# Kernel optimization log

Hardware: AMD Instinct MI355X
Metric: run time of the kernel (lower is better)

The kernel has to match this reference:

```python
import jax, jax.numpy as jnp
import numpy as np

NUM_SAMPLES = 128      # num_samples_per_ray
HIST_PAD = 0.01        # histogram_padding
EPS = 1e-5             # eps
N_RAYS = 262144
N_COARSE = 64


def setup_inputs() -> dict:
    key = jax.random.key(0)
    k1, k2 = jax.random.split(key, 2)
    weights = jax.random.uniform(k1, (N_RAYS, N_COARSE, 1), dtype=jnp.float32)
    # monotonically increasing bins along each ray (cumsum of positive deltas)
    deltas = jax.random.uniform(k2, (N_RAYS, N_COARSE + 1), dtype=jnp.float32) * 0.1 + 0.01
    t = jnp.cumsum(deltas, axis=-1)
    bins = t[:, :N_COARSE, None]        # [R, N, 1]
    max_bin = t[:, N_COARSE:]           # [R, 1]
    return {"weights": weights, "bins": bins, "max_bin": max_bin}


def reference(weights, bins, max_bin):
    # eval-mode PDFSampler (deterministic u = linspace + 0.5/num_bins)
    w = weights[..., 0] + HIST_PAD                      # [R, N]
    w_sum = jnp.sum(w, axis=-1, keepdims=True)          # [R, 1]
    padding = jnp.maximum(EPS - w_sum, 0.0)             # relu(eps - sum)
    w = w + padding / w.shape[-1]
    pdf = w / (w_sum + padding)
    cdf = jnp.minimum(jnp.cumsum(pdf, axis=-1), 1.0)    # clamp_max(1)
    cdf = jnp.concatenate([jnp.zeros_like(cdf[..., :1]), cdf], axis=-1)  # [R, N+1]

    num_bins = NUM_SAMPLES + 1
    u = jnp.linspace(0.0, 1.0 - 1.0 / num_bins, num_bins, dtype=cdf.dtype) + 0.5 / num_bins
    u = jnp.broadcast_to(u, (cdf.shape[0], num_bins))   # [R, S+1]

    existing_bins = jnp.concatenate([bins[..., 0], max_bin], axis=-1)  # [R, N+1]

    idx = jax.vmap(lambda c, uu: jnp.searchsorted(c, uu, side='right'))(cdf, u)
    last = cdf.shape[-1] - 1
    below = jnp.clip(idx - 1, 0, last)
    above = jnp.clip(idx, 0, last)

    cdf_g0 = jnp.take_along_axis(cdf, below, axis=-1)
    cdf_g1 = jnp.take_along_axis(cdf, above, axis=-1)
    bins_g0 = jnp.take_along_axis(existing_bins, below, axis=-1)
    bins_g1 = jnp.take_along_axis(existing_bins, above, axis=-1)

    denom = cdf_g1 - cdf_g0
    safe = jnp.where(denom > 0, denom, 1.0)
    ts = jnp.clip(jnp.where(denom > 0, (u - cdf_g0) / safe, 0.0), 0.0, 1.0)
    new_bins = bins_g0 + ts * (bins_g1 - bins_g0)       # [R, S+1]

    # include_original: merge with existing bins, sort, drop last
    new_bins = jnp.sort(jnp.concatenate([existing_bins, new_bins], axis=-1), axis=-1)[..., :-1]
    # [R, N + S + 1] = [R, 193]; caller splits into bins=new_bins[..., :-1, None], max_bin=new_bins[..., -1:]
    return new_bins
```

## Files before the change

kernel.cpp:

```cpp
#include <hip/hip_runtime.h>


constexpr int kNCoarse = 64;
constexpr int kNumU    = 129;
constexpr int kNOut    = 193;
constexpr int kWaves   = 8;
constexpr int kBlock   = kWaves * 64;
constexpr int kBlockF  = kWaves * kNOut;
constexpr int kBlockV4 = kBlockF / 4;

typedef float f32x4 __attribute__((ext_vector_type(4)));

#define DPP_UPD_F(oldv, srcv, ctrl, rmask, bctrl)                             \
  __int_as_float(__builtin_amdgcn_update_dpp(                                 \
      __float_as_int(oldv), __float_as_int(srcv), (ctrl), (rmask), 0xF, (bctrl)))

__global__ __launch_bounds__(kBlock) void pdf_sampler_kernel(
    const float* __restrict__ weights,
    const float* __restrict__ bins,
    const float* __restrict__ max_bin,
    float* __restrict__ out,
    int n_rays)
{
    const int tid  = threadIdx.x;
    const int lane = tid & 63;
    const int wid  = tid >> 6;
    const int ray  = blockIdx.x * kWaves + wid;

    __shared__ __align__(16) float s_m[kBlockF];

    if (ray < n_rays) {
        const float w  = weights[(size_t)ray * kNCoarse + lane] + 0.01f;
        const float b0 = bins[(size_t)ray * kNCoarse + lane];
        const float mb = max_bin[ray];

        float c = w;
        c += DPP_UPD_F(0.0f, c, 0x111, 0xF, true);
        c += DPP_UPD_F(0.0f, c, 0x112, 0xF, true);
        c += DPP_UPD_F(0.0f, c, 0x114, 0xF, true);
        c += DPP_UPD_F(0.0f, c, 0x118, 0xF, true);
        c += DPP_UPD_F(0.0f, c, 0x142, 0xA, false);
        c += DPP_UPD_F(0.0f, c, 0x143, 0xC, false);

        const float ws        = __int_as_float(__builtin_amdgcn_readlane(__float_as_int(c), 63));
        const float padding   = fmaxf(1e-5f - ws, 0.0f);
        const float inv_total = __builtin_amdgcn_rcpf(ws + padding);
        const float pad64     = padding * (1.0f / 64.0f);

        const float c1 = fminf((c + (float)(lane + 1) * pad64) * inv_total, 1.0f);
        const float c0 = DPP_UPD_F(0.0f, c1, 0x138, 0xF, true);
        const float b1 = DPP_UPD_F(mb,   b0, 0x130, 0xF, false);

        const float kInv = 1.0f / 129.0f, kHalf = 0.5f / 129.0f;
        int js = (int)ceilf(fmaf(c0, 129.0f, -0.5f));
        js = min(max(js, 0), kNumU);
        {
            const float um1 = fmaf((float)(js - 1), kInv, kHalf);
            const float u0e = fmaf((float)js,       kInv, kHalf);
            if (js > 0 && um1 >= c0)           js -= 1;
            else if (js < kNumU && u0e < c0)   js += 1;
        }
        const int js_next = __builtin_amdgcn_update_dpp(kNumU, js, 0x130, 0xF, 0xF, false);

        const float denom  = c1 - c0;
        const float rdenom = (denom > 0.0f) ? __builtin_amdgcn_rcpf(denom) : 0.0f;
        const float dbin   = b1 - b0;
        const float u0     = fmaf((float)js, kInv, kHalf);
        const float t0     = fminf(fmaxf((u0 - c0) * rdenom, 0.0f), 1.0f);
        float       val    = fmaf(t0, dbin, b0);
        const float step   = kInv * rdenom * dbin;

        float* mrow = s_m + wid * kNOut;
        mrow[lane + js] = b0;
        for (int j = js; j < js_next; ++j) {
            mrow[j + lane + 1] = val;
            val += step;
        }
    }

    __syncthreads();

    {
        const int raysHere = min(n_rays - blockIdx.x * kWaves, kWaves);
        if (raysHere > 0) {
            const int nf = raysHere * kNOut;
            float* obase = out + (size_t)blockIdx.x * kBlockF;
            if (tid < kBlockV4) {
                const int off = tid * 4;
                if (off + 3 < nf) {
                    const f32x4 v = *reinterpret_cast<const f32x4*>(&s_m[off]);
                    __builtin_nontemporal_store(v, reinterpret_cast<f32x4*>(&obase[off]));
                } else {
                    for (int k = off; k < nf; ++k)
                        __builtin_nontemporal_store(s_m[k], &obase[k]);
                }
            }
        }
    }
}

extern "C" void kernel_launch(void* const* d_in, const int* in_sizes, int n_in,
                              void* d_out, int out_size, void* d_ws, size_t ws_size,
                              hipStream_t stream) {
    const float* weights = (const float*)d_in[0];
    const float* bins    = (const float*)d_in[1];
    const float* max_bin = (const float*)d_in[2];
    float* out = (float*)d_out;
    const int n_rays = in_sizes[2];
    const int blocks = (n_rays + kWaves - 1) / kWaves;
    pdf_sampler_kernel<<<blocks, kBlock, 0, stream>>>(weights, bins, max_bin, out, n_rays);
}
```

Before: 55.70 us.

## Make kernel persistent with register prefetch and double-buffered LDS staging

Launches a fixed grid of 4096 blocks, and each block loops over a contiguous range of 8-ray groups. The next group's weights, bins and max_bin are loaded into registers while the current group is computed, and the output staging buffer in shared memory is double-buffered so only one barrier is needed per iteration. The aim is to cut block launch overhead and hide global load latency. In exchange, each block keeps fewer loads in flight per wave and carries a longer serial chain, and LDS use per block doubles.

```diff
diff --git a/kernel.cpp b/kernel.cpp
--- a/kernel.cpp
+++ b/kernel.cpp
@@ -6,8 +6,9 @@
 constexpr int kNOut    = 193;
 constexpr int kWaves   = 8;
 constexpr int kBlock   = kWaves * 64;
-constexpr int kBlockF  = kWaves * kNOut;
-constexpr int kBlockV4 = kBlockF / 4;
+constexpr int kGroupF  = kWaves * kNOut;
+constexpr int kGroupV4 = kGroupF / 4;
+constexpr int kGrid    = 4096;
 
 typedef float f32x4 __attribute__((ext_vector_type(4)));
 
@@ -25,74 +26,101 @@
     const int tid  = threadIdx.x;
     const int lane = tid & 63;
     const int wid  = tid >> 6;
-    const int ray  = blockIdx.x * kWaves + wid;
 
-    __shared__ __align__(16) float s_m[kBlockF];
+    const int nGroups = (n_rays + kWaves - 1) / kWaves;
+    const int T       = (nGroups + kGrid - 1) / kGrid;
+    const int g0      = blockIdx.x * T;
+    const int gEnd    = min(g0 + T, nGroups);
+    if (g0 >= nGroups) return;
 
-    if (ray < n_rays) {
-        const float w  = weights[(size_t)ray * kNCoarse + lane] + 0.01f;
-        const float b0 = bins[(size_t)ray * kNCoarse + lane];
-        const float mb = max_bin[ray];
+    __shared__ __align__(16) float s_m[2][kGroupF];
 
-        float c = w;
-        c += DPP_UPD_F(0.0f, c, 0x111, 0xF, true);
-        c += DPP_UPD_F(0.0f, c, 0x112, 0xF, true);
-        c += DPP_UPD_F(0.0f, c, 0x114, 0xF, true);
-        c += DPP_UPD_F(0.0f, c, 0x118, 0xF, true);
-        c += DPP_UPD_F(0.0f, c, 0x142, 0xA, false);
-        c += DPP_UPD_F(0.0f, c, 0x143, 0xC, false);
-
-        const float ws        = __int_as_float(__builtin_amdgcn_readlane(__float_as_int(c), 63));
-        const float padding   = fmaxf(1e-5f - ws, 0.0f);
-        const float inv_total = __builtin_amdgcn_rcpf(ws + padding);
-        const float pad64     = padding * (1.0f / 64.0f);
-
-        const float c1 = fminf((c + (float)(lane + 1) * pad64) * inv_total, 1.0f);
-        const float c0 = DPP_UPD_F(0.0f, c1, 0x138, 0xF, true);
-        const float b1 = DPP_UPD_F(mb,   b0, 0x130, 0xF, false);
-
-        const float kInv = 1.0f / 129.0f, kHalf = 0.5f / 129.0f;
-        int js = (int)ceilf(fmaf(c0, 129.0f, -0.5f));
-        js = min(max(js, 0), kNumU);
-        {
-            const float um1 = fmaf((float)(js - 1), kInv, kHalf);
-            const float u0e = fmaf((float)js,       kInv, kHalf);
-            if (js > 0 && um1 >= c0)           js -= 1;
-            else if (js < kNumU && u0e < c0)   js += 1;
-        }
-        const int js_next = __builtin_amdgcn_update_dpp(kNumU, js, 0x130, 0xF, 0xF, false);
-
-        const float denom  = c1 - c0;
-        const float rdenom = (denom > 0.0f) ? __builtin_amdgcn_rcpf(denom) : 0.0f;
-        const float dbin   = b1 - b0;
-        const float u0     = fmaf((float)js, kInv, kHalf);
-        const float t0     = fminf(fmaxf((u0 - c0) * rdenom, 0.0f), 1.0f);
-        float       val    = fmaf(t0, dbin, b0);
-        const float step   = kInv * rdenom * dbin;
-
-        float* mrow = s_m + wid * kNOut;
-        mrow[lane + js] = b0;
-        for (int j = js; j < js_next; ++j) {
-            mrow[j + lane + 1] = val;
-            val += step;
+    float w = 0.0f, b0 = 0.0f, mb = 0.0f;
+    {
+        const int ray = g0 * kWaves + wid;
+        if (ray < n_rays) {
+            w  = weights[(size_t)ray * kNCoarse + lane];
+            b0 = bins[(size_t)ray * kNCoarse + lane];
+            mb = max_bin[ray];
         }
     }
 
-    __syncthreads();
+    int p = 0;
+    for (int g = g0; g < gEnd; ++g, p ^= 1) {
+        const int ray = g * kWaves + wid;
 
-    {
-        const int raysHere = min(n_rays - blockIdx.x * kWaves, kWaves);
-        if (raysHere > 0) {
+        if (ray < n_rays) {
+            const float wp = w + 0.01f;
+
+            float c = wp;
+            c += DPP_UPD_F(0.0f, c, 0x111, 0xF, true);
+            c += DPP_UPD_F(0.0f, c, 0x112, 0xF, true);
+            c += DPP_UPD_F(0.0f, c, 0x114, 0xF, true);
+            c += DPP_UPD_F(0.0f, c, 0x118, 0xF, true);
+            c += DPP_UPD_F(0.0f, c, 0x142, 0xA, false);
+            c += DPP_UPD_F(0.0f, c, 0x143, 0xC, false);
+
+            const float ws        = __int_as_float(__builtin_amdgcn_readlane(__float_as_int(c), 63));
+            const float padding   = fmaxf(1e-5f - ws, 0.0f);
+            const float inv_total = __builtin_amdgcn_rcpf(ws + padding);
+            const float pad64     = padding * (1.0f / 64.0f);
+
+            const float c1 = fminf((c + (float)(lane + 1) * pad64) * inv_total, 1.0f);
+            const float c0 = DPP_UPD_F(0.0f, c1, 0x138, 0xF, true);
+            const float b1 = DPP_UPD_F(mb,   b0, 0x130, 0xF, false);
+
+            const float kInv = 1.0f / 129.0f, kHalf = 0.5f / 129.0f;
+            int js = (int)ceilf(fmaf(c0, 129.0f, -0.5f));
+            js = min(max(js, 0), kNumU);
+            {
+                const float um1 = fmaf((float)(js - 1), kInv, kHalf);
+                const float u0e = fmaf((float)js,       kInv, kHalf);
+                if (js > 0 && um1 >= c0)           js -= 1;
+                else if (js < kNumU && u0e < c0)   js += 1;
+            }
+            const int js_next = __builtin_amdgcn_update_dpp(kNumU, js, 0x130, 0xF, 0xF, false);
+
+            const float denom  = c1 - c0;
+            const float rdenom = (denom > 0.0f) ? __builtin_amdgcn_rcpf(denom) : 0.0f;
+            const float dbin   = b1 - b0;
+            const float u0     = fmaf((float)js, kInv, kHalf);
+            const float t0     = fminf(fmaxf((u0 - c0) * rdenom, 0.0f), 1.0f);
+            float       val    = fmaf(t0, dbin, b0);
+            const float step   = kInv * rdenom * dbin;
+
+            float* mrow = s_m[p] + wid * kNOut;
+            mrow[lane + js] = b0;
+            for (int j = js; j < js_next; ++j) {
+                mrow[j + lane + 1] = val;
+                val += step;
+            }
+        }
+
+        if (g + 1 < gEnd) {
+            const int nray = (g + 1) * kWaves + wid;
+            if (nray < n_rays) {
+                w  = weights[(size_t)nray * kNCoarse + lane];
+                b0 = bins[(size_t)nray * kNCoarse + lane];
+                mb = max_bin[nray];
+            } else {
+                w = 0.0f; b0 = 0.0f; mb = 0.0f;
+            }
+        }
+
+        __syncthreads();
+
+        {
+            const int raysHere = min(n_rays - g * kWaves, kWaves);
             const int nf = raysHere * kNOut;
-            float* obase = out + (size_t)blockIdx.x * kBlockF;
-            if (tid < kBlockV4) {
+            float* obase = out + (size_t)g * kGroupF;
+            if (tid < kGroupV4) {
                 const int off = tid * 4;
                 if (off + 3 < nf) {
-                    const f32x4 v = *reinterpret_cast<const f32x4*>(&s_m[off]);
+                    const f32x4 v = *reinterpret_cast<const f32x4*>(&s_m[p][off]);
                     __builtin_nontemporal_store(v, reinterpret_cast<f32x4*>(&obase[off]));
                 } else {
                     for (int k = off; k < nf; ++k)
-                        __builtin_nontemporal_store(s_m[k], &obase[k]);
+                        __builtin_nontemporal_store(s_m[p][k], &obase[k]);
                 }
             }
         }
@@ -107,6 +135,5 @@
     const float* max_bin = (const float*)d_in[2];
     float* out = (float*)d_out;
     const int n_rays = in_sizes[2];
-    const int blocks = (n_rays + kWaves - 1) / kWaves;
-    pdf_sampler_kernel<<<blocks, kBlock, 0, stream>>>(weights, bins, max_bin, out, n_rays);
+    pdf_sampler_kernel<<<kGrid, kBlock, 0, stream>>>(weights, bins, max_bin, out, n_rays);
 }
```

New measurement: 57.39 us. +3.0%, slower.
